# Optimization experiments

Hardware: AMD Instinct MI355X
Metric: run time of the kernel (lower is better)

Reference implementation:

```python
import jax, jax.numpy as jnp
import numpy as np

N, SB, SBR, Y, C, H, NBF = 5000, 49, 19, 2, 128, 256, 512
E = 10000


def setup_inputs() -> dict:
    key = jax.random.key(0)
    ks = jax.random.split(key, 12)
    s = lambda fan_in: 1.0 / np.sqrt(fan_in)
    return {
        "x": jax.random.normal(ks[0], (N, SB, C), jnp.float32),
        "x_edge": jax.random.normal(ks[1], (E, NBF), jnp.float32),
        "edge_index": jax.random.randint(ks[2], (2, E), 0, N, jnp.int64 if jax.config.jax_enable_x64 else jnp.int32),
        "wigner": jax.random.normal(ks[3], (E * Y, SBR, SB), jnp.float32) * s(SB),
        "wigner_inv": jax.random.normal(ks[4], (E, SB, SBR), jnp.float32) * s(SBR),
        "w_dist": jax.random.normal(ks[5], (NBF, H), jnp.float32) * s(NBF),
        "b_dist": jnp.zeros((H,), jnp.float32),
        "w_proj": jax.random.normal(ks[6], (2 * SBR * C, H), jnp.float32) * s(2 * SBR * C),
        "b_proj": jnp.zeros((H,), jnp.float32),
        "w_edge": jax.random.normal(ks[7], (H, H), jnp.float32) * s(H),
        "b_edge": jnp.zeros((H,), jnp.float32),
        "w_out": jax.random.normal(ks[8], (H, SBR * C), jnp.float32) * s(H),
        "b_out": jnp.zeros((SBR * C,), jnp.float32),
    }


def reference(x, x_edge, edge_index, wigner, wigner_inv,
              w_dist, b_dist, w_proj, b_proj, w_edge, b_edge, w_out, b_out):
    act = jax.nn.silu
    # distance embedding gate: [E, H]
    x_edge = act(x_edge @ w_dist + b_dist)
    # edge gathers: [E, SB, C]
    x_source = x[edge_index[0]]
    x_target = x[edge_index[1]]

    def rotate(v):
        # repeat each edge for Y y-rotations, then rotate with per-(edge,rot) Wigner matrix
        v = jnp.broadcast_to(v[:, None], (E, Y, SB, C)).reshape(E * Y, SB, C)
        r = jnp.einsum("ers,esc->erc", wigner, v)  # [E*Y, SBR, C]
        return r.reshape(E * Y, SBR * C)

    x_message = jnp.concatenate([rotate(x_source), rotate(x_target)], axis=1)  # [E*Y, 2*SBR*C]
    x_message = act(x_message @ w_proj + b_proj)  # [E*Y, H]
    # gate by distance embedding (broadcast over y rotations)
    x_message = (x_message.reshape(E, Y, H) * x_edge[:, None, :]).reshape(E * Y, H)
    x_message = act(x_message @ w_edge + b_edge)
    x_message = act(x_message @ w_out + b_out)  # [E*Y, SBR*C]
    # CombineYRotations: average over the Y rotated copies
    x_message = x_message.reshape(E, Y, SBR, C).mean(axis=1)  # [E, SBR, C]
    # RotateInv: back to full spherical basis per edge
    return jnp.einsum("ebs,esc->ebc", wigner_inv, x_message)  # [E, SB, C]
```

## Files before the change

### kernel.cpp

```cpp
#include <hip/hip_runtime.h>

#define E_N   10000
#define SB_N  49
#define SBR_N 19
#define C_N   128
#define H_N   256
#define NBF_N 512
#define KPROJ 4864
#define NOUT  2432
#define XB    64
#define KSPLIT 4
#define KCH   (KPROJ / KSPLIT)

typedef _Float16 f16x8 __attribute__((ext_vector_type(8)));
typedef _Float16 f16x4 __attribute__((ext_vector_type(4)));
typedef _Float16 f16x2 __attribute__((ext_vector_type(2)));
typedef float    f32x4 __attribute__((ext_vector_type(4)));

__device__ __forceinline__ float silu_f(float v) { return v / (1.0f + __expf(-v)); }

#define GLOBAL_PTR(p) ((const __attribute__((address_space(1))) void*)(p))
#define LDS_PTR(p)    ((__attribute__((address_space(3))) void*)(p))

__launch_bounds__(256)
__global__ void transpose_to_f16(const float* __restrict__ in, _Float16* __restrict__ out,
                                 int K, int N)
{
    __shared__ float tile[32][33];
    const int k0 = blockIdx.x * 32;
    const int n0 = blockIdx.y * 32;
    const int tx = threadIdx.x & 31;
    const int ty = threadIdx.x >> 5;
    #pragma unroll
    for (int i = ty; i < 32; i += 8)
        if (k0 + i < K && n0 + tx < N)
            tile[i][tx] = in[(size_t)(k0 + i) * N + (n0 + tx)];
    __syncthreads();
    #pragma unroll
    for (int i = ty; i < 32; i += 8)
        if (n0 + i < N && k0 + tx < K)
            out[(size_t)(n0 + i) * K + (k0 + tx)] = (_Float16)tile[tx][i];
}

__launch_bounds__(256)
__global__ void cvt_to_f16(const float* __restrict__ in, _Float16* __restrict__ out, int n4)
{
    int i = blockIdx.x * blockDim.x + threadIdx.x;
    const int stride = gridDim.x * blockDim.x;
    for (; i < n4; i += stride) {
        const float4 v = ((const float4*)in)[i];
        f16x4 o; o[0] = (_Float16)v.x; o[1] = (_Float16)v.y; o[2] = (_Float16)v.z; o[3] = (_Float16)v.w;
        ((f16x4*)out)[i] = o;
    }
}

__launch_bounds__(256)
__global__ void prep_xt(const float* __restrict__ x, _Float16* __restrict__ xt)
{
    __shared__ float xs[SB_N * C_N];
    const int n = blockIdx.x;
    const int tid = threadIdx.x;
    for (int t = tid; t < (SB_N * C_N) / 4; t += 256)
        ((float4*)xs)[t] = ((const float4*)(x + (size_t)n * (SB_N * C_N)))[t];
    __syncthreads();
    for (int t = tid; t < C_N * 8; t += 256) {
        const int c = t >> 3;
        const int slot = t & 7;
        const int kbase = (slot ^ (c & 7)) * 8;
        f16x8 v;
        #pragma unroll
        for (int j = 0; j < 8; ++j) {
            const int b = kbase + j;
            v[j] = (b < SB_N) ? (_Float16)xs[b * C_N + c] : (_Float16)0.f;
        }
        *(f16x8*)(xt + (size_t)n * (C_N * XB) + c * XB + slot * 8) = v;
    }
}

template<int GATED>
__launch_bounds__(256, 2)
__global__ void gemm_f16(const _Float16* __restrict__ A, int lda,
                         const _Float16* __restrict__ BT,
                         const float* __restrict__ bias,
                         const _Float16* __restrict__ gate,
                         _Float16* __restrict__ C,
                         int M, int N, int K, int i0)
{
    __shared__ __align__(16) _Float16 As[4][128][8];
    __shared__ __align__(16) _Float16 Bs[4][128][8];
    const int tid  = threadIdx.x;
    const int lane = tid & 63;
    const int w    = tid >> 6;
    const int wr   = w >> 1;
    const int wc   = w & 1;
    const int n0   = blockIdx.x * 128;
    const int m0   = blockIdx.y * 128;

    const int r01 = tid & 127;
    const int ks0 = tid >> 7;
    const int ks1 = ks0 + 2;
    const _Float16* a0 = A  + (size_t)(m0 + r01) * lda + ks0 * 8;
    const _Float16* a1 = A  + (size_t)(m0 + r01) * lda + ks1 * 8;
    const _Float16* b0 = BT + (size_t)(n0 + r01) * K   + ks0 * 8;
    const _Float16* b1 = BT + (size_t)(n0 + r01) * K   + ks1 * 8;
    _Float16* sA0 = &As[0][0][0] + (size_t)tid * 8;
    _Float16* sA1 = sA0 + 2048;
    _Float16* sB0 = &Bs[0][0][0] + (size_t)tid * 8;
    _Float16* sB1 = sB0 + 2048;

    const int frow = lane & 15;
    const int fks  = lane >> 4;
    const _Float16* fA = &As[fks][wr * 64 + frow][0];
    const _Float16* fB = &Bs[fks][wc * 64 + frow][0];

    f32x4 acc[4][4] = {};

    for (int k0 = 0; k0 < K; k0 += 32) {
        __builtin_amdgcn_global_load_lds(GLOBAL_PTR(a0 + k0), LDS_PTR(sA0), 16, 0, 0);
        __builtin_amdgcn_global_load_lds(GLOBAL_PTR(a1 + k0), LDS_PTR(sA1), 16, 0, 0);
        __builtin_amdgcn_global_load_lds(GLOBAL_PTR(b0 + k0), LDS_PTR(sB0), 16, 0, 0);
        __builtin_amdgcn_global_load_lds(GLOBAL_PTR(b1 + k0), LDS_PTR(sB1), 16, 0, 0);
        __syncthreads();
        f16x8 af[4], bf[4];
        #pragma unroll
        for (int m = 0; m < 4; ++m) af[m] = *(const f16x8*)(fA + m * 16 * 8);
        #pragma unroll
        for (int n = 0; n < 4; ++n) bf[n] = *(const f16x8*)(fB + n * 16 * 8);
        #pragma unroll
        for (int m = 0; m < 4; ++m)
            #pragma unroll
            for (int n = 0; n < 4; ++n)
                acc[m][n] = __builtin_amdgcn_mfma_f32_16x16x32_f16(af[m], bf[n], acc[m][n], 0, 0, 0);
        __syncthreads();
    }

    #pragma unroll
    for (int m = 0; m < 4; ++m) {
        #pragma unroll
        for (int n = 0; n < 4; ++n) {
            const int gn = n0 + wc * 64 + n * 16 + (lane & 15);
            #pragma unroll
            for (int r = 0; r < 4; ++r) {
                const int gm = m0 + wr * 64 + m * 16 + (lane >> 4) * 4 + r;
                if (gm < M) {
                    float v = acc[m][n][r] + bias[gn];
                    v = silu_f(v);
                    if (GATED) v *= (float)gate[(size_t)((i0 + gm) >> 1) * H_N + gn];
                    C[(size_t)gm * N + gn] = (_Float16)v;
                }
            }
        }
    }
}

__launch_bounds__(256, 2)
__global__ void gemm_f16_splitk(const _Float16* __restrict__ A, int lda,
                                const _Float16* __restrict__ BT,
                                float* __restrict__ partial, size_t pstride,
                                int N)
{
    __shared__ __align__(16) _Float16 As[4][128][8];
    __shared__ __align__(16) _Float16 Bs[4][128][8];
    const int tid  = threadIdx.x;
    const int lane = tid & 63;
    const int w    = tid >> 6;
    const int wr   = w >> 1;
    const int wc   = w & 1;
    const int n0   = blockIdx.x * 128;
    const int m0   = blockIdx.y * 128;
    const int kspl = blockIdx.z;

    const int r01 = tid & 127;
    const int ks0 = tid >> 7;
    const int ks1 = ks0 + 2;
    const _Float16* a0 = A  + (size_t)(m0 + r01) * lda + kspl * KCH + ks0 * 8;
    const _Float16* a1 = A  + (size_t)(m0 + r01) * lda + kspl * KCH + ks1 * 8;
    const _Float16* b0 = BT + (size_t)(n0 + r01) * KPROJ + kspl * KCH + ks0 * 8;
    const _Float16* b1 = BT + (size_t)(n0 + r01) * KPROJ + kspl * KCH + ks1 * 8;
    _Float16* sA0 = &As[0][0][0] + (size_t)tid * 8;
    _Float16* sA1 = sA0 + 2048;
    _Float16* sB0 = &Bs[0][0][0] + (size_t)tid * 8;
    _Float16* sB1 = sB0 + 2048;

    const int frow = lane & 15;
    const int fks  = lane >> 4;
    const _Float16* fA = &As[fks][wr * 64 + frow][0];
    const _Float16* fB = &Bs[fks][wc * 64 + frow][0];

    f32x4 acc[4][4] = {};

    for (int k0 = 0; k0 < KCH; k0 += 32) {
        __builtin_amdgcn_global_load_lds(GLOBAL_PTR(a0 + k0), LDS_PTR(sA0), 16, 0, 0);
        __builtin_amdgcn_global_load_lds(GLOBAL_PTR(a1 + k0), LDS_PTR(sA1), 16, 0, 0);
        __builtin_amdgcn_global_load_lds(GLOBAL_PTR(b0 + k0), LDS_PTR(sB0), 16, 0, 0);
        __builtin_amdgcn_global_load_lds(GLOBAL_PTR(b1 + k0), LDS_PTR(sB1), 16, 0, 0);
        __syncthreads();
        f16x8 af[4], bf[4];
        #pragma unroll
        for (int m = 0; m < 4; ++m) af[m] = *(const f16x8*)(fA + m * 16 * 8);
        #pragma unroll
        for (int n = 0; n < 4; ++n) bf[n] = *(const f16x8*)(fB + n * 16 * 8);
        #pragma unroll
        for (int m = 0; m < 4; ++m)
            #pragma unroll
            for (int n = 0; n < 4; ++n)
                acc[m][n] = __builtin_amdgcn_mfma_f32_16x16x32_f16(af[m], bf[n], acc[m][n], 0, 0, 0);
        __syncthreads();
    }

    float* pout = partial + (size_t)kspl * pstride;
    #pragma unroll
    for (int m = 0; m < 4; ++m) {
        #pragma unroll
        for (int n = 0; n < 4; ++n) {
            const int gn = n0 + wc * 64 + n * 16 + (lane & 15);
            #pragma unroll
            for (int r = 0; r < 4; ++r) {
                const int gm = m0 + wr * 64 + m * 16 + (lane >> 4) * 4 + r;
                pout[(size_t)gm * N + gn] = acc[m][n][r];
            }
        }
    }
}

__launch_bounds__(256)
__global__ void reduce_silu_gate(const float* __restrict__ partial, size_t pstride,
                                 const float* __restrict__ bias,
                                 const _Float16* __restrict__ gate,
                                 _Float16* __restrict__ h1, int ci, int i0)
{
    const int total = ci * (H_N / 4);
    const int gstride = gridDim.x * blockDim.x;
    for (int idx = blockIdx.x * blockDim.x + threadIdx.x; idx < total; idx += gstride) {
        const int m = idx >> 6;
        const int n = (idx & 63) * 4;
        const size_t off = (size_t)m * H_N + n;
        const float4 p0 = *(const float4*)(partial + 0 * pstride + off);
        const float4 p1 = *(const float4*)(partial + 1 * pstride + off);
        const float4 p2 = *(const float4*)(partial + 2 * pstride + off);
        const float4 p3 = *(const float4*)(partial + 3 * pstride + off);
        const float4 bi = *(const float4*)(bias + n);
        const f16x4 g = *(const f16x4*)(gate + (size_t)((i0 + m) >> 1) * H_N + n);
        f16x4 o;
        float v;
        v = p0.x + p1.x + p2.x + p3.x + bi.x; v = silu_f(v) * (float)g[0]; o[0] = (_Float16)v;
        v = p0.y + p1.y + p2.y + p3.y + bi.y; v = silu_f(v) * (float)g[1]; o[1] = (_Float16)v;
        v = p0.z + p1.z + p2.z + p3.z + bi.z; v = silu_f(v) * (float)g[2]; o[2] = (_Float16)v;
        v = p0.w + p1.w + p2.w + p3.w + bi.w; v = silu_f(v) * (float)g[3]; o[3] = (_Float16)v;
        *(f16x4*)(h1 + off) = o;
    }
}

__launch_bounds__(256, 4)
__global__ void rotate_v3(const _Float16* __restrict__ xt, const float* __restrict__ wigner,
                          const int* __restrict__ eidx, _Float16* __restrict__ rot, int e0)
{
    __shared__ __align__(16) _Float16 xs[2][C_N][XB];
    __shared__ __align__(16) _Float16 wg[48][XB];
    const int tid = threadIdx.x;
    const int e = e0 + blockIdx.x;
    const int node0 = eidx[e];
    const int node1 = eidx[E_N + e];

    const _Float16* p0 = xt + (size_t)node0 * (C_N * XB);
    const _Float16* p1 = xt + (size_t)node1 * (C_N * XB);
    _Float16* d0 = &xs[0][0][0] + tid * 8;
    _Float16* d1 = &xs[1][0][0] + tid * 8;
    #pragma unroll
    for (int ch = 0; ch < 4; ++ch) {
        __builtin_amdgcn_global_load_lds(GLOBAL_PTR(p0 + ch * 2048 + tid * 8), LDS_PTR(d0 + ch * 2048), 16, 0, 0);
        __builtin_amdgcn_global_load_lds(GLOBAL_PTR(p1 + ch * 2048 + tid * 8), LDS_PTR(d1 + ch * 2048), 16, 0, 0);
    }

    {
        f16x8 z = {};
        for (int t = tid; t < (48 * XB) / 8; t += 256)
            *(f16x8*)(&wg[0][0] + t * 8) = z;
    }
    __syncthreads();
    const float* wsrc = wigner + (size_t)(2 * e) * (SBR_N * SB_N);
    for (int t = tid; t < 2 * SBR_N * SB_N; t += 256) {
        const int y = (t >= SBR_N * SB_N);
        const int sb = t - y * (SBR_N * SB_N);
        const int s = sb / SB_N, b = sb - s * SB_N;
        const int row = y * SBR_N + s;
        const int idx = ((b >> 3) ^ (row & 7)) * 8 + (b & 7);
        wg[row][idx] = (_Float16)wsrc[t];
    }
    __syncthreads();

    const int lane = tid & 63;
    const int w = tid >> 6;
    const int part = w >> 1;
    const int nh = w & 1;
    const int frow = lane & 15;
    const int fks = lane >> 4;

    f16x8 af[3][2];
    #pragma unroll
    for (int mt = 0; mt < 3; ++mt) {
        const int row = mt * 16 + frow;
        #pragma unroll
        for (int kt = 0; kt < 2; ++kt) {
            const int slot = (kt * 4 + fks) ^ (row & 7);
            af[mt][kt] = *(const f16x8*)&wg[row][slot * 8];
        }
    }

    f32x4 acc[3][4] = {};
    #pragma unroll
    for (int nt = 0; nt < 4; ++nt) {
        const int n = nh * 64 + nt * 16 + frow;
        #pragma unroll
        for (int kt = 0; kt < 2; ++kt) {
            const int slot = (kt * 4 + fks) ^ (n & 7);
            const f16x8 bf = *(const f16x8*)&xs[part][n][slot * 8];
            #pragma unroll
            for (int mt = 0; mt < 3; ++mt)
                acc[mt][nt] = __builtin_amdgcn_mfma_f32_16x16x32_f16(af[mt][kt], bf, acc[mt][nt], 0, 0, 0);
        }
    }

    const size_t rowbase = 2 * (size_t)blockIdx.x;
    #pragma unroll
    for (int mt = 0; mt < 3; ++mt) {
        #pragma unroll
        for (int rr = 0; rr < 4; ++rr) {
            const int m = mt * 16 + (lane >> 4) * 4 + rr;
            if (m < 2 * SBR_N) {
                const int y = (m >= SBR_N);
                const int s = m - y * SBR_N;
                _Float16* orow = rot + (rowbase + y) * KPROJ + part * NOUT + s * C_N
                               + nh * 64 + (lane & 15);
                #pragma unroll
                for (int nt = 0; nt < 4; ++nt)
                    orow[nt * 16] = (_Float16)acc[mt][nt][rr];
            }
        }
    }
}

__launch_bounds__(128)
__global__ void combine_kernel(const _Float16* __restrict__ h3, const float* __restrict__ wigner_inv,
                               float* __restrict__ out, int e0)
{
    __shared__ float ms[SBR_N * C_N];
    __shared__ float wv[SB_N * SBR_N];
    const int eb = blockIdx.x;
    const int e = e0 + eb;
    const int c = threadIdx.x;

    #pragma unroll
    for (int s = 0; s < SBR_N; ++s) {
        const float a = (float)h3[(size_t)(2 * eb) * NOUT + s * C_N + c];
        const float b = (float)h3[(size_t)(2 * eb + 1) * NOUT + s * C_N + c];
        ms[s * C_N + c] = 0.5f * (a + b);
    }
    for (int t = c; t < SB_N * SBR_N; t += 128)
        wv[t] = wigner_inv[(size_t)e * (SB_N * SBR_N) + t];
    __syncthreads();

    for (int b = 0; b < SB_N; ++b) {
        float acc = 0.f;
        #pragma unroll
        for (int s = 0; s < SBR_N; ++s)
            acc += wv[b * SBR_N + s] * ms[s * C_N + c];
        out[(size_t)e * (SB_N * C_N) + b * C_N + c] = acc;
    }
}

extern "C" void kernel_launch(void* const* d_in, const int* in_sizes, int n_in,
                              void* d_out, int out_size, void* d_ws, size_t ws_size,
                              hipStream_t stream)
{
    const float* x          = (const float*)d_in[0];
    const float* x_edge     = (const float*)d_in[1];
    const int*   eidx       = (const int*)d_in[2];
    const float* wigner     = (const float*)d_in[3];
    const float* wigner_inv = (const float*)d_in[4];
    const float* w_dist     = (const float*)d_in[5];
    const float* b_dist     = (const float*)d_in[6];
    const float* w_proj     = (const float*)d_in[7];
    const float* b_proj     = (const float*)d_in[8];
    const float* w_edge     = (const float*)d_in[9];
    const float* b_edge     = (const float*)d_in[10];
    const float* w_out      = (const float*)d_in[11];
    const float* b_out      = (const float*)d_in[12];
    float* out = (float*)d_out;

    char* wsp = (char*)d_ws;
    auto alloc = [&](size_t bytes) -> char* {
        char* p = wsp;
        wsp += (bytes + 255) & ~(size_t)255;
        return p;
    };
    const int XE_ROWS = 10112;
    _Float16* gate = (_Float16*)alloc((size_t)E_N * H_N * sizeof(_Float16));
    _Float16* wTd  = (_Float16*)alloc((size_t)H_N * NBF_N * sizeof(_Float16));
    _Float16* wTp  = (_Float16*)alloc((size_t)H_N * KPROJ * sizeof(_Float16));
    _Float16* wTe  = (_Float16*)alloc((size_t)H_N * H_N * sizeof(_Float16));
    _Float16* wTo  = (_Float16*)alloc((size_t)NOUT * H_N * sizeof(_Float16));
    _Float16* xeh  = (_Float16*)alloc((size_t)XE_ROWS * NBF_N * sizeof(_Float16));
    _Float16* xt   = (_Float16*)alloc((size_t)5000 * C_N * XB * sizeof(_Float16));

    const size_t used = (size_t)(wsp - (char*)d_ws);
    const size_t avail = ws_size > used ? ws_size - used : 0;
    const size_t per_row = (size_t)(KPROJ + H_N + H_N) * sizeof(_Float16)
                         + (size_t)KSPLIT * H_N * sizeof(float);
    long cimax = (long)(avail / per_row) & ~127L;
    if (cimax > 20096) cimax = 20096;
    if (cimax < 128) cimax = 128;

    _Float16* rot  = (_Float16*)alloc((size_t)cimax * KPROJ * sizeof(_Float16));
    _Float16* h1   = (_Float16*)alloc((size_t)cimax * H_N * sizeof(_Float16));
    _Float16* h2   = (_Float16*)alloc((size_t)cimax * H_N * sizeof(_Float16));
    float*    part = (float*)alloc((size_t)KSPLIT * cimax * H_N * sizeof(float));
    const size_t pstride = (size_t)cimax * H_N;

    transpose_to_f16<<<dim3(NBF_N / 32, H_N / 32), 256, 0, stream>>>(w_dist, wTd, NBF_N, H_N);
    transpose_to_f16<<<dim3(KPROJ / 32, H_N / 32), 256, 0, stream>>>(w_proj, wTp, KPROJ, H_N);
    transpose_to_f16<<<dim3(H_N / 32, H_N / 32), 256, 0, stream>>>(w_edge, wTe, H_N, H_N);
    transpose_to_f16<<<dim3(H_N / 32, NOUT / 32), 256, 0, stream>>>(w_out, wTo, H_N, NOUT);
    cvt_to_f16<<<dim3(1024), 256, 0, stream>>>(x_edge, xeh, (E_N * NBF_N) / 4);
    prep_xt<<<dim3(5000), 256, 0, stream>>>(x, xt);

    gemm_f16<0><<<dim3(H_N / 128, XE_ROWS / 128), 256, 0, stream>>>(
        xeh, NBF_N, wTd, b_dist, nullptr, gate, E_N, H_N, NBF_N, 0);

    for (long i0 = 0; i0 < 2L * E_N; i0 += cimax) {
        long ci = 2L * E_N - i0;
        if (ci > cimax) ci = cimax;
        const unsigned cb = (unsigned)((ci + 127) / 128);

        rotate_v3<<<dim3((unsigned)(ci / 2)), 256, 0, stream>>>(
            xt, wigner, eidx, rot, (int)(i0 / 2));

        gemm_f16_splitk<<<dim3(H_N / 128, cb, KSPLIT), 256, 0, stream>>>(
            rot, KPROJ, wTp, part, pstride, H_N);

        {
            const int total = (int)ci * (H_N / 4);
            unsigned rb = (unsigned)((total + 255) / 256);
            if (rb > 2048) rb = 2048;
            reduce_silu_gate<<<dim3(rb), 256, 0, stream>>>(
                part, pstride, b_proj, gate, h1, (int)ci, (int)i0);
        }

        gemm_f16<0><<<dim3(H_N / 128, cb), 256, 0, stream>>>(
            h1, H_N, wTe, b_edge, nullptr, h2, (int)ci, H_N, H_N, 0);

        gemm_f16<0><<<dim3(NOUT / 128, cb), 256, 0, stream>>>(
            h2, H_N, wTo, b_out, nullptr, rot, (int)ci, NOUT, H_N, 0);

        combine_kernel<<<dim3((unsigned)(ci / 2)), 128, 0, stream>>>(
            rot, wigner_inv, out, (int)(i0 / 2));
    }
}
```

Measured before the change: 964.3 us.

## Triple-buffer LDS tiles in f16 GEMM kernels to overlap global loads with MFMA

Both GEMM kernels (plain and split-K) now use a three-stage LDS ring buffer filled by async global_load_lds. Loads for future k-tiles are issued before computing the current one, and explicit vmcnt waits with raw barriers replace the per-iteration __syncthreads pairs. The aim is to hide global memory latency behind MFMA work. In exchange, shared memory per block triples to 48KB, which may limit occupancy, and correctness now depends on hand-written waitcnt counts and requires at least two k-tiles.

Result: no change. 961.2 us (-0.3%).

```diff
diff --git a/kernel.cpp b/kernel.cpp
--- a/kernel.cpp
+++ b/kernel.cpp
@@ -77,6 +77,56 @@
     }
 }
 
+#define PIPE_STAGE(BUF, KOFF) do {                                                            \
+    _Float16* sa_ = &As[BUF][0][0][0] + tid * 8;                                              \
+    _Float16* sb_ = &Bs[BUF][0][0][0] + tid * 8;                                              \
+    __builtin_amdgcn_global_load_lds(GLOBAL_PTR(a0 + (KOFF)), LDS_PTR(sa_),        16, 0, 0); \
+    __builtin_amdgcn_global_load_lds(GLOBAL_PTR(a1 + (KOFF)), LDS_PTR(sa_ + 2048), 16, 0, 0); \
+    __builtin_amdgcn_global_load_lds(GLOBAL_PTR(b0 + (KOFF)), LDS_PTR(sb_),        16, 0, 0); \
+    __builtin_amdgcn_global_load_lds(GLOBAL_PTR(b1 + (KOFF)), LDS_PTR(sb_ + 2048), 16, 0, 0); \
+} while (0)
+
+#define PIPE_COMPUTE(BUF) do {                                                          \
+    const _Float16* fA_ = &As[BUF][fks][wr * 64 + frow][0];                             \
+    const _Float16* fB_ = &Bs[BUF][fks][wc * 64 + frow][0];                             \
+    f16x8 af[4], bf[4];                                                                 \
+    _Pragma("unroll")                                                                   \
+    for (int m_ = 0; m_ < 4; ++m_) af[m_] = *(const f16x8*)(fA_ + m_ * 128);            \
+    _Pragma("unroll")                                                                   \
+    for (int n_ = 0; n_ < 4; ++n_) bf[n_] = *(const f16x8*)(fB_ + n_ * 128);            \
+    _Pragma("unroll")                                                                   \
+    for (int m_ = 0; m_ < 4; ++m_)                                                      \
+        _Pragma("unroll")                                                               \
+        for (int n_ = 0; n_ < 4; ++n_)                                                  \
+            acc[m_][n_] = __builtin_amdgcn_mfma_f32_16x16x32_f16(af[m_], bf[n_], acc[m_][n_], 0, 0, 0); \
+} while (0)
+
+#define PIPE_KLOOP(NT, KSTRIDE) do {                                                    \
+    PIPE_STAGE(0, 0);                                                                   \
+    PIPE_STAGE(1, (KSTRIDE));                                                           \
+    int cur_ = 0;                                                                       \
+    int koff_ = 2 * (KSTRIDE);                                                          \
+    for (int t_ = 0; t_ < (NT) - 2; ++t_) {                                             \
+        const int fut_ = cur_ >= 1 ? cur_ - 1 : 2;                       \
+        PIPE_STAGE(fut_, koff_); koff_ += (KSTRIDE);                                    \
+        asm volatile("s_waitcnt vmcnt(8)" ::: "memory");                                \
+        __builtin_amdgcn_s_barrier();                                                   \
+        __builtin_amdgcn_sched_barrier(0);                                              \
+        PIPE_COMPUTE(cur_);                                                             \
+        __builtin_amdgcn_s_barrier();                                                   \
+        cur_ = cur_ < 2 ? cur_ + 1 : 0;                                                 \
+    }                                                                                   \
+    asm volatile("s_waitcnt vmcnt(4)" ::: "memory");                                    \
+    __builtin_amdgcn_s_barrier();                                                       \
+    __builtin_amdgcn_sched_barrier(0);                                                  \
+    PIPE_COMPUTE(cur_);                                                                 \
+    cur_ = cur_ < 2 ? cur_ + 1 : 0;                                                     \
+    asm volatile("s_waitcnt vmcnt(0)" ::: "memory");                                    \
+    __builtin_amdgcn_s_barrier();                                                       \
+    __builtin_amdgcn_sched_barrier(0);                                                  \
+    PIPE_COMPUTE(cur_);                                                                 \
+} while (0)
+
 template<int GATED>
 __launch_bounds__(256, 2)
 __global__ void gemm_f16(const _Float16* __restrict__ A, int lda,
@@ -86,8 +136,8 @@
                          _Float16* __restrict__ C,
                          int M, int N, int K, int i0)
 {
-    __shared__ __align__(16) _Float16 As[4][128][8];
-    __shared__ __align__(16) _Float16 Bs[4][128][8];
+    __shared__ __align__(16) _Float16 As[3][4][128][8];
+    __shared__ __align__(16) _Float16 Bs[3][4][128][8];
     const int tid  = threadIdx.x;
     const int lane = tid & 63;
     const int w    = tid >> 6;
@@ -103,36 +153,13 @@
     const _Float16* a1 = A  + (size_t)(m0 + r01) * lda + ks1 * 8;
     const _Float16* b0 = BT + (size_t)(n0 + r01) * K   + ks0 * 8;
     const _Float16* b1 = BT + (size_t)(n0 + r01) * K   + ks1 * 8;
-    _Float16* sA0 = &As[0][0][0] + (size_t)tid * 8;
-    _Float16* sA1 = sA0 + 2048;
-    _Float16* sB0 = &Bs[0][0][0] + (size_t)tid * 8;
-    _Float16* sB1 = sB0 + 2048;
 
     const int frow = lane & 15;
     const int fks  = lane >> 4;
-    const _Float16* fA = &As[fks][wr * 64 + frow][0];
-    const _Float16* fB = &Bs[fks][wc * 64 + frow][0];
 
     f32x4 acc[4][4] = {};
-
-    for (int k0 = 0; k0 < K; k0 += 32) {
-        __builtin_amdgcn_global_load_lds(GLOBAL_PTR(a0 + k0), LDS_PTR(sA0), 16, 0, 0);
-        __builtin_amdgcn_global_load_lds(GLOBAL_PTR(a1 + k0), LDS_PTR(sA1), 16, 0, 0);
-        __builtin_amdgcn_global_load_lds(GLOBAL_PTR(b0 + k0), LDS_PTR(sB0), 16, 0, 0);
-        __builtin_amdgcn_global_load_lds(GLOBAL_PTR(b1 + k0), LDS_PTR(sB1), 16, 0, 0);
-        __syncthreads();
-        f16x8 af[4], bf[4];
-        #pragma unroll
-        for (int m = 0; m < 4; ++m) af[m] = *(const f16x8*)(fA + m * 16 * 8);
-        #pragma unroll
-        for (int n = 0; n < 4; ++n) bf[n] = *(const f16x8*)(fB + n * 16 * 8);
-        #pragma unroll
-        for (int m = 0; m < 4; ++m)
-            #pragma unroll
-            for (int n = 0; n < 4; ++n)
-                acc[m][n] = __builtin_amdgcn_mfma_f32_16x16x32_f16(af[m], bf[n], acc[m][n], 0, 0, 0);
-        __syncthreads();
-    }
+    const int nt = K >> 5;
+    PIPE_KLOOP(nt, 32);
 
     #pragma unroll
     for (int m = 0; m < 4; ++m) {
@@ -159,8 +186,8 @@
                                 float* __restrict__ partial, size_t pstride,
                                 int N)
 {
-    __shared__ __align__(16) _Float16 As[4][128][8];
-    __shared__ __align__(16) _Float16 Bs[4][128][8];
+    __shared__ __align__(16) _Float16 As[3][4][128][8];
+    __shared__ __align__(16) _Float16 Bs[3][4][128][8];
     const int tid  = threadIdx.x;
     const int lane = tid & 63;
     const int w    = tid >> 6;
@@ -177,36 +204,12 @@
     const _Float16* a1 = A  + (size_t)(m0 + r01) * lda + kspl * KCH + ks1 * 8;
     const _Float16* b0 = BT + (size_t)(n0 + r01) * KPROJ + kspl * KCH + ks0 * 8;
     const _Float16* b1 = BT + (size_t)(n0 + r01) * KPROJ + kspl * KCH + ks1 * 8;
-    _Float16* sA0 = &As[0][0][0] + (size_t)tid * 8;
-    _Float16* sA1 = sA0 + 2048;
-    _Float16* sB0 = &Bs[0][0][0] + (size_t)tid * 8;
-    _Float16* sB1 = sB0 + 2048;
 
     const int frow = lane & 15;
     const int fks  = lane >> 4;
-    const _Float16* fA = &As[fks][wr * 64 + frow][0];
-    const _Float16* fB = &Bs[fks][wc * 64 + frow][0];
 
     f32x4 acc[4][4] = {};
-
-    for (int k0 = 0; k0 < KCH; k0 += 32) {
-        __builtin_amdgcn_global_load_lds(GLOBAL_PTR(a0 + k0), LDS_PTR(sA0), 16, 0, 0);
-        __builtin_amdgcn_global_load_lds(GLOBAL_PTR(a1 + k0), LDS_PTR(sA1), 16, 0, 0);
-        __builtin_amdgcn_global_load_lds(GLOBAL_PTR(b0 + k0), LDS_PTR(sB0), 16, 0, 0);
-        __builtin_amdgcn_global_load_lds(GLOBAL_PTR(b1 + k0), LDS_PTR(sB1), 16, 0, 0);
-        __syncthreads();
-        f16x8 af[4], bf[4];
-        #pragma unroll
-        for (int m = 0; m < 4; ++m) af[m] = *(const f16x8*)(fA + m * 16 * 8);
-        #pragma unroll
-        for (int n = 0; n < 4; ++n) bf[n] = *(const f16x8*)(fB + n * 16 * 8);
-        #pragma unroll
-        for (int m = 0; m < 4; ++m)
-            #pragma unroll
-            for (int n = 0; n < 4; ++n)
-                acc[m][n] = __builtin_amdgcn_mfma_f32_16x16x32_f16(af[m], bf[n], acc[m][n], 0, 0, 0);
-        __syncthreads();
-    }
+    PIPE_KLOOP(KCH / 32, 32);
 
     float* pout = partial + (size_t)kspl * pstride;
     #pragma unroll
```
